# Kernel tuning notes

Hardware: AMD Instinct MI355X
Metric: run time of the kernel (lower is better)

The kernel has to match this reference:

```python
import jax, jax.numpy as jnp
import numpy as np

EPS_BN = 1e-5
EPS_NORM = 1e-12

def _proj(x, W, g, b, m, v):
    # x: (B,C,N); W: (O,C) 1x1 conv; eval-mode BN per out channel; ReLU
    y = jnp.einsum('oc,bcn->bon', W, x)
    s = g / jnp.sqrt(v + EPS_BN)
    y = (y - m[None, :, None]) * s[None, :, None] + b[None, :, None]
    return jax.nn.relu(y)

def _l2norm(x, axis):
    n = jnp.sqrt(jnp.sum(x * x, axis=axis, keepdims=True))
    return x / jnp.maximum(n, EPS_NORM)

def setup_inputs() -> dict:
    key = jax.random.key(0)
    ks = jax.random.split(key, 8)
    B, C, H, W = 8, 256, 96, 96
    NS, K = 256, 64  # num_state, K
    X = jax.random.normal(ks[0], (B, C, H, W), dtype=jnp.float32)
    def mk(k, out_c):
        return (jax.random.normal(k, (out_c, C), dtype=jnp.float32) * 0.05,
                jnp.ones((out_c,), jnp.float32), jnp.zeros((out_c,), jnp.float32),
                jnp.zeros((out_c,), jnp.float32), jnp.ones((out_c,), jnp.float32))
    phi_w, phi_g, phi_b, phi_m, phi_v = mk(ks[1], K)
    theta_w, theta_g, theta_b, theta_m, theta_v = mk(ks[2], NS)
    rou_w, rou_g, rou_b, rou_m, rou_v = mk(ks[3], NS)
    val_w, val_g, val_b, val_m, val_v = mk(ks[4], NS)
    return dict(X=X,
                phi_w=phi_w, phi_g=phi_g, phi_b=phi_b, phi_m=phi_m, phi_v=phi_v,
                theta_w=theta_w, theta_g=theta_g, theta_b=theta_b, theta_m=theta_m, theta_v=theta_v,
                rou_w=rou_w, rou_g=rou_g, rou_b=rou_b, rou_m=rou_m, rou_v=rou_v,
                val_w=val_w, val_g=val_g, val_b=val_b, val_m=val_m, val_v=val_v)

def reference(X, phi_w, phi_g, phi_b, phi_m, phi_v,
              theta_w, theta_g, theta_b, theta_m, theta_v,
              rou_w, rou_g, rou_b, rou_m, rou_v,
              val_w, val_g, val_b, val_m, val_v):
    B, C, H, W = X.shape
    N = H * W
    x = X.reshape(B, C, N)
    x_phi = _proj(x, phi_w, phi_g, phi_b, phi_m, phi_v)          # (B,K,N)
    x_theta = _proj(x, theta_w, theta_g, theta_b, theta_m, theta_v)  # (B,S,N)
    x_theta = jax.nn.softmax(x_theta, axis=-1)                   # softmax over N
    discrib = jnp.einsum('bkn,bsn->bks', x_phi, x_theta)         # (B,K,S)
    x_rou = _proj(x, rou_w, rou_g, rou_b, rou_m, rou_v)          # (B,S,N)
    x_rou = jax.nn.softmax(x_rou, axis=1)                        # softmax over channels S
    Q = jnp.einsum('bks,bsn->bnk', discrib, x_rou)               # (B,N,K)
    Q = _l2norm(Q, axis=1)                                       # F.normalize dim=1 (over N)
    Q = jax.nn.softmax(Q, axis=-1)                               # softmax over K
    x_val = _proj(x, val_w, val_g, val_b, val_m, val_v)          # (B,S,N)
    # Z = sum_n Q[b,n,k]*x_val[b,s,n] / sum_n Q[b,n,k]  -- batched GEMM, no (B,S,N,K) blowup
    Znum = jnp.einsum('bsn,bnk->bsk', x_val, Q)                  # (B,S,K)
    Z = Znum / Q.sum(axis=1)[:, None, :]
    Z = _l2norm(Z, axis=1)                                       # F.normalize dim=1 (over S)
    return (Z, Q)
```

## Files before the change

### kernel.cpp

```cpp
#include <hip/hip_runtime.h>
#include <math.h>

#define B_ 8
#define C_ 256
#define N_ 9216
#define S_ 256
#define K_ 64
#define NCHUNK 36
#define TILE_KS (K_ * S_)
#define NC8 (N_ / 8)

typedef unsigned short ushort_t;
typedef __attribute__((ext_vector_type(8))) short bf16x8;
typedef __attribute__((ext_vector_type(4))) float f32x4;

static __device__ inline ushort_t f2bf(float x) {
    unsigned int u = __float_as_uint(x);
    unsigned int r = (u + 0x7fffu + ((u >> 16) & 1u)) >> 16;
    return (ushort_t)r;
}
static __device__ inline float bf2f(ushort_t u) {
    return __uint_as_float(((unsigned int)u) << 16);
}

static __device__ inline uint4 expcell(uint4 u, float2 s) {
    uint4 r;
    unsigned int* up = (unsigned int*)&u;
    unsigned int* rp = (unsigned int*)&r;
#pragma unroll
    for (int q = 0; q < 4; ++q) {
        unsigned int x = up[q];
        float lo = __uint_as_float((x & 0xffffu) << 16);
        float hi = __uint_as_float(x & 0xffff0000u);
        float el = __expf(lo - s.x) * s.y;
        float eh = __expf(hi - s.x) * s.y;
        rp[q] = (unsigned int)f2bf(el) | ((unsigned int)f2bf(eh) << 16);
    }
    return r;
}

__global__ __launch_bounds__(256) void prep_w(
    const float* __restrict__ phi_w, const float* __restrict__ phi_g, const float* __restrict__ phi_b,
    const float* __restrict__ phi_m, const float* __restrict__ phi_v,
    const float* __restrict__ th_w, const float* __restrict__ th_g, const float* __restrict__ th_b,
    const float* __restrict__ th_m, const float* __restrict__ th_v,
    const float* __restrict__ ro_w, const float* __restrict__ ro_g, const float* __restrict__ ro_b,
    const float* __restrict__ ro_m, const float* __restrict__ ro_v,
    const float* __restrict__ va_w, const float* __restrict__ va_g, const float* __restrict__ va_b,
    const float* __restrict__ va_m, const float* __restrict__ va_v,
    ushort_t* __restrict__ Wt, float* __restrict__ be)
{
    const int o = blockIdx.x;
    const int t = threadIdx.x;
    const float *src, *g, *bb, *mm, *vv; int orel;
    if (o < 64)       { src = phi_w; g = phi_g; bb = phi_b; mm = phi_m; vv = phi_v; orel = o; }
    else if (o < 320) { src = th_w;  g = th_g;  bb = th_b;  mm = th_m;  vv = th_v;  orel = o - 64; }
    else if (o < 576) { src = ro_w;  g = ro_g;  bb = ro_b;  mm = ro_m;  vv = ro_v;  orel = o - 320; }
    else              { src = va_w;  g = va_g;  bb = va_b;  mm = va_m;  vv = va_v;  orel = o - 576; }
    const float s = g[orel] / sqrtf(vv[orel] + 1e-5f);
    const int ot = o >> 6, os = (o >> 4) & 3, st = t >> 5;
    const size_t flat = ((((size_t)ot * 8 + st) * 4 + os) * 64 + ((t >> 3) & 3) * 16 + (o & 15)) * 8 + (t & 7);
    Wt[flat] = f2bf(src[orel * C_ + t] * s);
    if (t == 0) be[o] = bb[orel] - mm[orel] * s;
}

__global__ __launch_bounds__(256) void xpose(
    const float* __restrict__ X, ushort_t* __restrict__ Xs)
{
    __shared__ float T[64][65];
    const int b = blockIdx.z, c0 = blockIdx.y * 64, n0 = blockIdx.x * 64;
    const int t = threadIdx.x;
#pragma unroll
    for (int p = 0; p < 4; ++p) {
        int c = p * 16 + (t >> 4), nn = (t & 15) * 4;
        float4 v = *(const float4*)&X[((size_t)b * C_ + c0 + c) * N_ + n0 + nn];
        T[c][nn] = v.x; T[c][nn + 1] = v.y; T[c][nn + 2] = v.z; T[c][nn + 3] = v.w;
    }
    __syncthreads();
#pragma unroll
    for (int p = 0; p < 4; ++p) {
        int nn = p * 16 + (t >> 4), cl = (t & 15) * 4;
        ushort4 u;
        u.x = f2bf(T[cl][nn]); u.y = f2bf(T[cl + 1][nn]);
        u.z = f2bf(T[cl + 2][nn]); u.w = f2bf(T[cl + 3][nn]);
        const int n = n0 + nn, c = c0 + cl;
        const int nt = n >> 8, nr = n & 255;
        const int st = c >> 5, g8 = (c >> 3) & 3, e = c & 7;
        const size_t base = ((((size_t)b * 36 + nt) * 8 + st) * 1024
                             + (nr >> 4) * 64 + g8 * 16 + (nr & 15)) * 8 + e;
        *(ushort4*)&Xs[base] = u;
    }
}

__global__ __launch_bounds__(256) void proj_mfma_all(
    const ushort_t* __restrict__ Wt, const float* __restrict__ be,
    const ushort_t* __restrict__ Xs,
    ushort_t* __restrict__ Pbf, ushort_t* __restrict__ Tbf,
    ushort_t* __restrict__ Vbf, ushort_t* __restrict__ Rt)
{
    __shared__ short sm[9216];
    const int t = threadIdx.x;
    const int l = t & 63, w = t >> 6;
    const int idx = blockIdx.x;
    const int xcd = idx & 7, pos = idx >> 3;
    const int vid = xcd * 468 + pos;
    const int ot  = vid % 13;
    const int r   = vid / 13;
    const int b   = r / 36;
    const int nt  = r % 36;
    const int n0  = nt * 256;
    const int o0  = ot * 64;

    const bf16x8* Wv = (const bf16x8*)Wt;
    const bf16x8* Xf = (const bf16x8*)Xs;
    const size_t xbase = ((size_t)b * 36 + nt) * 8192;
    const size_t wbase = (size_t)ot * 2048;
    const int boff = (l >> 4) * 16 + (l & 15);

    f32x4 zr = {0.f, 0.f, 0.f, 0.f};
    f32x4 acc[4][4];
#pragma unroll
    for (int i = 0; i < 4; ++i)
#pragma unroll
        for (int j = 0; j < 4; ++j) acc[i][j] = zr;

    bf16x8 A0[4], B0[4];
#pragma unroll
    for (int os = 0; os < 4; ++os) A0[os] = Wv[wbase + os * 64 + l];
#pragma unroll
    for (int j = 0; j < 4; ++j)   B0[j]  = Xf[xbase + (w * 4 + j) * 64 + boff];

#pragma unroll
    for (int st = 0; st < 8; ++st) {
        bf16x8 A1[4], B1[4];
        if (st < 7) {
#pragma unroll
            for (int os = 0; os < 4; ++os)
                A1[os] = Wv[wbase + (st + 1) * 256 + os * 64 + l];
#pragma unroll
            for (int j = 0; j < 4; ++j)
                B1[j] = Xf[xbase + (size_t)(st + 1) * 1024 + (w * 4 + j) * 64 + boff];
        }
#pragma unroll
        for (int os = 0; os < 4; ++os)
#pragma unroll
            for (int j = 0; j < 4; ++j)
                acc[os][j] = __builtin_amdgcn_mfma_f32_16x16x32_bf16(A0[os], B0[j], acc[os][j], 0, 0, 0);
#pragma unroll
        for (int os = 0; os < 4; ++os) A0[os] = A1[os];
#pragma unroll
        for (int j = 0; j < 4; ++j)   B0[j]  = B1[j];
    }

    if (o0 >= 320 && o0 < 576) {
        const int od = o0 - 320;
        ushort_t* Tt = (ushort_t*)sm + w * (32 * 72);
#pragma unroll
        for (int half = 0; half < 2; ++half) {
            __syncthreads();
#pragma unroll
            for (int jj = 0; jj < 2; ++jj) {
                const int j = half * 2 + jj;
#pragma unroll
                for (int os = 0; os < 4; ++os)
#pragma unroll
                    for (int r2 = 0; r2 < 4; ++r2) {
                        const int scol = os * 16 + (l >> 4) * 4 + r2;
                        const float bias = be[o0 + scol];
                        Tt[(jj * 16 + (l & 15)) * 72 + scol] = f2bf(fmaxf(acc[os][j][r2] + bias, 0.f));
                    }
            }
            __syncthreads();
#pragma unroll
            for (int p = 0; p < 4; ++p) {
                const int lrow = p * 8 + (l >> 3);
                uint4 v = *(const uint4*)&Tt[lrow * 72 + (l & 7) * 8];
                *(uint4*)&Rt[((size_t)b * N_ + n0 + w * 64 + half * 32 + lrow) * 256 + od + (l & 7) * 8] = v;
            }
        }
    } else {
        ushort_t* dst; int od, osz;
        if (o0 < 64)       { dst = Pbf; od = o0;       osz = 64;  }
        else if (o0 < 320) { dst = Tbf; od = o0 - 64;  osz = 256; }
        else               { dst = Vbf; od = o0 - 576; osz = 256; }
        ushort_t* Tw = (ushort_t*)sm + w * (32 * 68);
#pragma unroll
        for (int half = 0; half < 2; ++half) {
            __syncthreads();
#pragma unroll
            for (int osl = 0; osl < 2; ++osl) {
                const int os = half * 2 + osl;
#pragma unroll
                for (int r2 = 0; r2 < 4; ++r2) {
                    const int lrow = osl * 16 + (l >> 4) * 4 + r2;
                    const int orow = half * 32 + lrow;
                    const float bias = be[o0 + orow];
#pragma unroll
                    for (int j = 0; j < 4; ++j)
                        Tw[lrow * 68 + j * 16 + (l & 15)] = f2bf(fmaxf(acc[os][j][r2] + bias, 0.f));
                }
            }
            __syncthreads();
#pragma unroll
            for (int i = 0; i < 8; ++i) {
                const int lrow = i * 4 + (l >> 4);
                ushort4 v = *(const ushort4*)&Tw[lrow * 68 + (l & 15) * 4];
                *(ushort4*)&dst[((size_t)(b * osz + od + half * 32 + lrow)) * N_ + n0 + w * 64 + (l & 15) * 4] = v;
            }
        }
    }
}

__global__ __launch_bounds__(256) void rowstat_n(
    const ushort_t* __restrict__ T, float* __restrict__ st2)
{
    const int row = blockIdx.x;
    const ushort4* p = (const ushort4*)(T + (size_t)row * N_);
    const int t = threadIdx.x;
    float v[36];
    float mx = -INFINITY;
#pragma unroll
    for (int i = 0; i < 9; ++i) {
        ushort4 u = p[t + i * 256];
        v[i * 4 + 0] = bf2f(u.x); v[i * 4 + 1] = bf2f(u.y);
        v[i * 4 + 2] = bf2f(u.z); v[i * 4 + 3] = bf2f(u.w);
        mx = fmaxf(mx, fmaxf(fmaxf(v[i * 4], v[i * 4 + 1]), fmaxf(v[i * 4 + 2], v[i * 4 + 3])));
    }
    __shared__ float red[256];
    red[t] = mx; __syncthreads();
    for (int s2 = 128; s2 > 0; s2 >>= 1) {
        if (t < s2) red[t] = fmaxf(red[t], red[t + s2]);
        __syncthreads();
    }
    mx = red[0]; __syncthreads();
    float sum = 0.f;
#pragma unroll
    for (int i = 0; i < 36; ++i) sum += __expf(v[i] - mx);
    red[t] = sum; __syncthreads();
    for (int s2 = 128; s2 > 0; s2 >>= 1) {
        if (t < s2) red[t] += red[t + s2];
        __syncthreads();
    }
    if (t == 0) ((float2*)st2)[row] = make_float2(mx, 1.0f / red[0]);
}

__global__ __launch_bounds__(256) void softmax_rows(ushort_t* __restrict__ R)
{
    const int w = threadIdx.x >> 6, l = threadIdx.x & 63;
    const size_t row0 = (size_t)blockIdx.x * 32 + w * 8;
    for (int r = 0; r < 8; ++r) {
        ushort4* p = (ushort4*)(R + (row0 + r) * 256);
        ushort4 u = p[l];
        float f0 = bf2f(u.x), f1 = bf2f(u.y), f2 = bf2f(u.z), f3 = bf2f(u.w);
        float mx = fmaxf(fmaxf(f0, f1), fmaxf(f2, f3));
#pragma unroll
        for (int m = 1; m < 64; m <<= 1) mx = fmaxf(mx, __shfl_xor(mx, m));
        f0 = __expf(f0 - mx); f1 = __expf(f1 - mx); f2 = __expf(f2 - mx); f3 = __expf(f3 - mx);
        float s = f0 + f1 + f2 + f3;
#pragma unroll
        for (int m = 1; m < 64; m <<= 1) s += __shfl_xor(s, m);
        const float inv = 1.0f / s;
        u.x = f2bf(f0 * inv); u.y = f2bf(f1 * inv); u.z = f2bf(f2 * inv); u.w = f2bf(f3 * inv);
        p[l] = u;
    }
}

__global__ __launch_bounds__(256) void ks_mfma(
    const ushort_t* __restrict__ A, const ushort_t* __restrict__ Bm,
    const float* __restrict__ st2, float* __restrict__ P)
{
    __shared__ short sm[32768];
    const int t = threadIdx.x;
    const int l = t & 63, w = t >> 6;
    const int chunk = blockIdx.x, b = blockIdx.y;
    const int ccell = chunk * 32;

    const uint4* Av = (const uint4*)A;
    const uint4* Bv = (const uint4*)Bm;
    const float2* S2 = (const float2*)st2;
    uint4* smv = (uint4*)sm;
    const bool doexp = (st2 != nullptr);

    uint4 wreg[8], xreg[8];
    float2 sreg[8];
#pragma unroll
    for (int i = 0; i < 8; ++i) {
        int cell = i * 256 + t;
        int osub = cell >> 9, g = (cell >> 4) & 31, oi = cell & 15;
        wreg[i] = Av[(size_t)(b * 64 + osub * 16 + oi) * NC8 + ccell + g];
    }
#pragma unroll
    for (int i = 0; i < 8; ++i) {
        int cell = i * 256 + t;
        int s = cell >> 7, g8 = (cell >> 4) & 7, ni = cell & 15;
        int row = s * 16 + ni;
        xreg[i] = Bv[(size_t)(b * 256 + row) * NC8 + ccell + g8];
        if (doexp) sreg[i] = S2[b * 256 + row];
    }
#pragma unroll
    for (int i = 0; i < 8; ++i) smv[i * 256 + t] = wreg[i];
#pragma unroll
    for (int i = 0; i < 8; ++i) smv[2048 + i * 256 + t] = doexp ? expcell(xreg[i], sreg[i]) : xreg[i];
    __syncthreads();

    f32x4 zr = {0.f, 0.f, 0.f, 0.f};
    f32x4 acc[4][4];
#pragma unroll
    for (int i = 0; i < 4; ++i)
#pragma unroll
        for (int j = 0; j < 4; ++j) acc[i][j] = zr;

    const bf16x8* smW = (const bf16x8*)sm;
    const bf16x8* smX = (const bf16x8*)(sm + 16384);

    for (int st = 0; st < 4; ++st) {
        if (st < 3) {
#pragma unroll
            for (int i = 0; i < 8; ++i) {
                int cell = i * 256 + t;
                int s = cell >> 7, g8 = (cell >> 4) & 7, ni = cell & 15;
                int row = s * 16 + ni;
                xreg[i] = Bv[(size_t)(b * 256 + row) * NC8 + ccell + (st + 1) * 8 + g8];
                if (doexp) sreg[i] = S2[b * 256 + row];
            }
        }
#pragma unroll
        for (int kgl = 0; kgl < 2; ++kgl) {
            const int kg = st * 2 + kgl;
            bf16x8 Af[4], Bf[4];
#pragma unroll
            for (int os = 0; os < 4; ++os)
                Af[os] = smW[(os * 32 + kg * 4 + (l >> 4)) * 16 + (l & 15)];
#pragma unroll
            for (int j = 0; j < 4; ++j)
                Bf[j] = smX[((w * 4 + j) * 8 + kgl * 4 + (l >> 4)) * 16 + (l & 15)];
#pragma unroll
            for (int os = 0; os < 4; ++os)
#pragma unroll
                for (int j = 0; j < 4; ++j)
                    acc[os][j] = __builtin_amdgcn_mfma_f32_16x16x32_bf16(Af[os], Bf[j], acc[os][j], 0, 0, 0);
        }
        __syncthreads();
        if (st < 3) {
#pragma unroll
            for (int i = 0; i < 8; ++i) smv[2048 + i * 256 + t] = doexp ? expcell(xreg[i], sreg[i]) : xreg[i];
            __syncthreads();
        }
    }

    float* Pb = P + ((size_t)(chunk * B_ + b)) * TILE_KS;
#pragma unroll
    for (int os = 0; os < 4; ++os)
#pragma unroll
        for (int r = 0; r < 4; ++r) {
            const int k = os * 16 + (l >> 4) * 4 + r;
#pragma unroll
            for (int j = 0; j < 4; ++j)
                Pb[k * 256 + (w * 4 + j) * 16 + (l & 15)] = acc[os][j][r];
        }
}

__global__ __launch_bounds__(256) void qt_mfma(
    const ushort_t* __restrict__ Dbf,
    const ushort_t* __restrict__ Rsm,
    float* __restrict__ Qraw,
    float* __restrict__ Nrm)
{
    __shared__ short sm[32768];
    const int t = threadIdx.x;
    const int l = t & 63, w = t >> 6;
    const int b = blockIdx.x / 36;
    const int n0 = (blockIdx.x % 36) * 256;

    const uint4* Av = (const uint4*)Dbf;
    const uint4* Xv = (const uint4*)Rsm;
    uint4* smv = (uint4*)sm;

    uint4 wreg[8], xreg[8];
#pragma unroll
    for (int i = 0; i < 8; ++i) {
        int cell = i * 256 + t;
        int osub = cell >> 9, g = (cell >> 4) & 31, oi = cell & 15;
        wreg[i] = Av[(size_t)(b * 64 + osub * 16 + oi) * 32 + g];
    }
#pragma unroll
    for (int i = 0; i < 8; ++i) {
        int cell = i * 256 + t;
        int s = cell >> 7, g8 = (cell >> 4) & 7, ni = cell & 15;
        xreg[i] = Xv[((size_t)b * N_ + n0 + s * 16 + ni) * 32 + g8];
    }
#pragma unroll
    for (int i = 0; i < 8; ++i) smv[i * 256 + t] = wreg[i];
#pragma unroll
    for (int i = 0; i < 8; ++i) smv[2048 + i * 256 + t] = xreg[i];
    __syncthreads();

    f32x4 zr = {0.f, 0.f, 0.f, 0.f};
    f32x4 acc[4][4];
#pragma unroll
    for (int i = 0; i < 4; ++i)
#pragma unroll
        for (int j = 0; j < 4; ++j) acc[i][j] = zr;

    const bf16x8* smW = (const bf16x8*)sm;
    const bf16x8* smX = (const bf16x8*)(sm + 16384);

    for (int st = 0; st < 4; ++st) {
        if (st < 3) {
#pragma unroll
            for (int i = 0; i < 8; ++i) {
                int cell = i * 256 + t;
                int s = cell >> 7, g8 = (cell >> 4) & 7, ni = cell & 15;
                xreg[i] = Xv[((size_t)b * N_ + n0 + s * 16 + ni) * 32 + (st + 1) * 8 + g8];
            }
        }
#pragma unroll
        for (int kgl = 0; kgl < 2; ++kgl) {
            const int kg = st * 2 + kgl;
            bf16x8 Af[4], Bf[4];
#pragma unroll
            for (int os = 0; os < 4; ++os)
                Af[os] = smW[(os * 32 + kg * 4 + (l >> 4)) * 16 + (l & 15)];
#pragma unroll
            for (int j = 0; j < 4; ++j)
                Bf[j] = smX[((w * 4 + j) * 8 + kgl * 4 + (l >> 4)) * 16 + (l & 15)];
#pragma unroll
            for (int os = 0; os < 4; ++os)
#pragma unroll
                for (int j = 0; j < 4; ++j)
                    acc[os][j] = __builtin_amdgcn_mfma_f32_16x16x32_bf16(Af[os], Bf[j], acc[os][j], 0, 0, 0);
        }
        __syncthreads();
        if (st < 3) {
#pragma unroll
            for (int i = 0; i < 8; ++i) smv[2048 + i * 256 + t] = xreg[i];
            __syncthreads();
        }
    }

    float* snrm = (float*)sm + 9216;
    __syncthreads();
    if (t < 64) snrm[t] = 0.f;
    __syncthreads();
#pragma unroll
    for (int os = 0; os < 4; ++os)
#pragma unroll
        for (int r = 0; r < 4; ++r) {
            float p = 0.f;
#pragma unroll
            for (int j = 0; j < 4; ++j) p = fmaf(acc[os][j][r], acc[os][j][r], p);
#pragma unroll
            for (int m = 1; m < 16; m <<= 1) p += __shfl_xor(p, m);
            if ((l & 15) == 0) atomicAdd(&snrm[os * 16 + (l >> 4) * 4 + r], p);
        }
    float* Tw = (float*)sm + w * 2304;
#pragma unroll
    for (int h = 0; h < 2; ++h) {
        __syncthreads();
#pragma unroll
        for (int os = 0; os < 4; ++os)
#pragma unroll
            for (int r = 0; r < 4; ++r) {
                const int kcol = os * 16 + (l >> 4) * 4 + r;
#pragma unroll
                for (int jj = 0; jj < 2; ++jj)
                    Tw[(jj * 16 + (l & 15)) * 72 + kcol] = acc[os][h * 2 + jj][r];
            }
        __syncthreads();
#pragma unroll
        for (int i = 0; i < 8; ++i) {
            const int lrow = i * 4 + (l >> 4);
            f32x4 v = *(const f32x4*)&Tw[lrow * 72 + (l & 15) * 4];
            *(f32x4*)&Qraw[((size_t)b * N_ + n0 + w * 64 + h * 32 + lrow) * 64 + (l & 15) * 4] = v;
        }
    }
    __syncthreads();
    if (t < 64) atomicAdd(&Nrm[b * 64 + t], snrm[t]);
}

__global__ __launch_bounds__(256) void chunk_reduce_bf(
    const float* __restrict__ P, ushort_t* __restrict__ outb)
{
    const int i = blockIdx.x * 256 + threadIdx.x;
    float s = 0.f;
#pragma unroll
    for (int c = 0; c < NCHUNK; ++c) s += P[(size_t)c * (B_ * TILE_KS) + i];
    outb[i] = f2bf(s);
}
__global__ __launch_bounds__(256) void chunk_reduce_f(
    const float* __restrict__ P, float* __restrict__ outf)
{
    const int i = blockIdx.x * 256 + threadIdx.x;
    float s = 0.f;
#pragma unroll
    for (int c = 0; c < NCHUNK; ++c) s += P[(size_t)c * (B_ * TILE_KS) + i];
    outf[i] = s;
}

__global__ __launch_bounds__(256) void q_final(
    const float* __restrict__ Qraw, const float* __restrict__ Nrm,
    float* __restrict__ Qout, ushort_t* __restrict__ Qbf)
{
    __shared__ ushort_t Tq[64 * 256];
    __shared__ float invn[64];
    const int b = blockIdx.y;
    const int n0 = blockIdx.x * 256;
    const int t = threadIdx.x;
    const int l = t & 63, w = t >> 6;
    if (t < 64) invn[t] = 1.0f / fmaxf(sqrtf(Nrm[b * 64 + t]), 1e-12f);
    __syncthreads();
    const size_t base = ((size_t)b * N_ + n0 + t) * 64;
    float q[64];
#pragma unroll
    for (int kk = 0; kk < 16; ++kk) {
        f32x4 v = *(const f32x4*)&Qraw[base + kk * 4];
        q[kk * 4 + 0] = v[0]; q[kk * 4 + 1] = v[1]; q[kk * 4 + 2] = v[2]; q[kk * 4 + 3] = v[3];
    }
    float mx = -INFINITY;
#pragma unroll
    for (int k = 0; k < 64; ++k) { q[k] *= invn[k]; mx = fmaxf(mx, q[k]); }
    float sum = 0.f;
#pragma unroll
    for (int k = 0; k < 64; ++k) { q[k] = __expf(q[k] - mx); sum += q[k]; }
    const float inv = 1.0f / sum;
#pragma unroll
    for (int kk = 0; kk < 16; ++kk) {
        f32x4 v = {q[kk * 4] * inv, q[kk * 4 + 1] * inv, q[kk * 4 + 2] * inv, q[kk * 4 + 3] * inv};
        *(f32x4*)&Qout[base + kk * 4] = v;
        q[kk * 4] = v[0]; q[kk * 4 + 1] = v[1]; q[kk * 4 + 2] = v[2]; q[kk * 4 + 3] = v[3];
    }
#pragma unroll
    for (int k = 0; k < 64; ++k) Tq[k * 256 + t] = f2bf(q[k]);
    __syncthreads();
#pragma unroll
    for (int kk = 0; kk < 16; ++kk) {
        const int k = kk * 4 + w;
        ushort4 v = *(const ushort4*)&Tq[k * 256 + l * 4];
        *(ushort4*)&Qbf[((size_t)b * 64 + k) * N_ + n0 + l * 4] = v;
    }
}

__global__ __launch_bounds__(256) void z_final(
    const float* __restrict__ ZnT, float* __restrict__ Z)
{
    __shared__ float red[256];
    __shared__ float invn[64];
    const int b = blockIdx.x;
    const int t = threadIdx.x;
    const float* Zb = ZnT + (size_t)b * TILE_KS;
    {
        const int k = t >> 2, qq = t & 3;
        float ss = 0.f;
        for (int j = 0; j < 64; ++j) {
            float v = Zb[k * 256 + qq * 64 + j];
            ss = fmaf(v, v, ss);
        }
        red[t] = ss;
    }
    __syncthreads();
    if ((t & 3) == 0) {
        float tot = red[t] + red[t + 1] + red[t + 2] + red[t + 3];
        invn[t >> 2] = 1.0f / fmaxf(sqrtf(tot), 1e-12f);
    }
    __syncthreads();
    {
        const int k = t & 63, w = t >> 6;
        const float sc = invn[k];
        for (int j = 0; j < 64; ++j) {
            int s = w * 64 + j;
            Z[((size_t)b * 256 + s) * 64 + k] = Zb[k * 256 + s] * sc;
        }
    }
}

extern "C" void kernel_launch(void* const* d_in, const int* in_sizes, int n_in,
                              void* d_out, int out_size, void* d_ws, size_t ws_size,
                              hipStream_t stream)
{
    const float* X       = (const float*)d_in[0];
    const float* phi_w   = (const float*)d_in[1];
    const float* phi_g   = (const float*)d_in[2];
    const float* phi_b   = (const float*)d_in[3];
    const float* phi_m   = (const float*)d_in[4];
    const float* phi_v   = (const float*)d_in[5];
    const float* theta_w = (const float*)d_in[6];
    const float* theta_g = (const float*)d_in[7];
    const float* theta_b = (const float*)d_in[8];
    const float* theta_m = (const float*)d_in[9];
    const float* theta_v = (const float*)d_in[10];
    const float* rou_w   = (const float*)d_in[11];
    const float* rou_g   = (const float*)d_in[12];
    const float* rou_b   = (const float*)d_in[13];
    const float* rou_m   = (const float*)d_in[14];
    const float* rou_v   = (const float*)d_in[15];
    const float* val_w   = (const float*)d_in[16];
    const float* val_g   = (const float*)d_in[17];
    const float* val_b   = (const float*)d_in[18];
    const float* val_m   = (const float*)d_in[19];
    const float* val_v   = (const float*)d_in[20];

    float* ws = (float*)d_ws;
    size_t off = 0;
    ushort_t* Xs  = (ushort_t*)(ws + off); off += (size_t)B_ * N_ * C_ / 2;
    ushort_t* Wt  = (ushort_t*)(ws + off); off += 832 * C_ / 2;
    float* be     = ws + off; off += 832;
    float* st2    = ws + off; off += 2 * B_ * 256;
    ushort_t* Pbf = (ushort_t*)(ws + off); off += (size_t)B_ * 64 * N_ / 2;
    ushort_t* Tbf = (ushort_t*)(ws + off); off += (size_t)B_ * 256 * N_ / 2;
    ushort_t* Vbf = (ushort_t*)(ws + off); off += (size_t)B_ * 256 * N_ / 2;
    ushort_t* Rt  = (ushort_t*)(ws + off); off += (size_t)B_ * N_ * 256 / 2;
    ushort_t* Qbf = (ushort_t*)(ws + off); off += (size_t)B_ * 64 * N_ / 2;
    ushort_t* Dbf = (ushort_t*)(ws + off); off += (size_t)B_ * 64 * 256 / 2;
    float* part   = ws + off; off += (size_t)NCHUNK * B_ * TILE_KS;
    float* Qraw   = ws + off; off += (size_t)B_ * N_ * 64;
    float* ZnT    = ws + off; off += (size_t)B_ * TILE_KS;
    float* Nrm    = ws + off; off += B_ * 64;

    float* Zout = (float*)d_out;
    float* Qout = Zout + (size_t)B_ * S_ * K_;

    hipMemsetAsync(Nrm, 0, B_ * 64 * sizeof(float), stream);

    prep_w<<<832, 256, 0, stream>>>(phi_w, phi_g, phi_b, phi_m, phi_v,
                                    theta_w, theta_g, theta_b, theta_m, theta_v,
                                    rou_w, rou_g, rou_b, rou_m, rou_v,
                                    val_w, val_g, val_b, val_m, val_v, Wt, be);
    xpose<<<dim3(N_ / 64, C_ / 64, B_), 256, 0, stream>>>(X, Xs);

    proj_mfma_all<<<3744, 256, 0, stream>>>(Wt, be, Xs, Pbf, Tbf, Vbf, Rt);

    rowstat_n<<<B_ * 256, 256, 0, stream>>>(Tbf, st2);
    softmax_rows<<<B_ * N_ / 32, 256, 0, stream>>>(Rt);

    ks_mfma<<<dim3(NCHUNK, B_), 256, 0, stream>>>(Pbf, Tbf, st2, part);
    chunk_reduce_bf<<<B_ * TILE_KS / 256, 256, 0, stream>>>(part, Dbf);

    qt_mfma<<<36 * B_, 256, 0, stream>>>(Dbf, Rt, Qraw, Nrm);
    q_final<<<dim3(36, B_), 256, 0, stream>>>(Qraw, Nrm, Qout, Qbf);

    ks_mfma<<<dim3(NCHUNK, B_), 256, 0, stream>>>(Qbf, Vbf, (const float*)nullptr, part);
    chunk_reduce_f<<<B_ * TILE_KS / 256, 256, 0, stream>>>(part, ZnT);
    z_final<<<B_, 256, 0, stream>>>(ZnT, Zout);
}
```

Before: 233.1 us.

## Defer channel softmax into qt_mfma, use packed bf16 converts, vectorize chunk reductions

The channel softmax over Rt is split: a new rowstat_rt kernel writes only per-row max and reciprocal-sum, and qt_mfma applies exp and scale while staging tiles into shared memory, so the normalized bf16 write-back of Rt is gone. Scalar bf16 rounding is replaced by the hardware packed v_cvt_pk_bf16_f32 instruction in xpose, the projection epilogues and expcell. The chunk_reduce kernels now handle four elements per thread with float4 loads. The trade is extra exp work inside qt_mfma, an added per-row stats buffer, and one fewer rounding step for the softmax values.

```diff
diff --git a/kernel.cpp b/kernel.cpp
--- a/kernel.cpp
+++ b/kernel.cpp
@@ -22,6 +22,11 @@
 static __device__ inline float bf2f(ushort_t u) {
     return __uint_as_float(((unsigned int)u) << 16);
 }
+static __device__ inline unsigned int cvtpk(float lo, float hi) {
+    unsigned int r;
+    asm("v_cvt_pk_bf16_f32 %0, %1, %2" : "=v"(r) : "v"(lo), "v"(hi));
+    return r;
+}
 
 static __device__ inline uint4 expcell(uint4 u, float2 s) {
     uint4 r;
@@ -32,9 +37,7 @@
         unsigned int x = up[q];
         float lo = __uint_as_float((x & 0xffffu) << 16);
         float hi = __uint_as_float(x & 0xffff0000u);
-        float el = __expf(lo - s.x) * s.y;
-        float eh = __expf(hi - s.x) * s.y;
-        rp[q] = (unsigned int)f2bf(el) | ((unsigned int)f2bf(eh) << 16);
+        rp[q] = cvtpk(__expf(lo - s.x) * s.y, __expf(hi - s.x) * s.y);
     }
     return r;
 }
@@ -80,15 +83,15 @@
 #pragma unroll
     for (int p = 0; p < 4; ++p) {
         int nn = p * 16 + (t >> 4), cl = (t & 15) * 4;
-        ushort4 u;
-        u.x = f2bf(T[cl][nn]); u.y = f2bf(T[cl + 1][nn]);
-        u.z = f2bf(T[cl + 2][nn]); u.w = f2bf(T[cl + 3][nn]);
+        uint2 uu;
+        uu.x = cvtpk(T[cl][nn], T[cl + 1][nn]);
+        uu.y = cvtpk(T[cl + 2][nn], T[cl + 3][nn]);
         const int n = n0 + nn, c = c0 + cl;
         const int nt = n >> 8, nr = n & 255;
         const int st = c >> 5, g8 = (c >> 3) & 3, e = c & 7;
         const size_t base = ((((size_t)b * 36 + nt) * 8 + st) * 1024
                              + (nr >> 4) * 64 + g8 * 16 + (nr & 15)) * 8 + e;
-        *(ushort4*)&Xs[base] = u;
+        *(uint2*)&Xs[base] = uu;
     }
 }
 
@@ -161,14 +164,19 @@
 #pragma unroll
             for (int jj = 0; jj < 2; ++jj) {
                 const int j = half * 2 + jj;
-#pragma unroll
-                for (int os = 0; os < 4; ++os)
-#pragma unroll
-                    for (int r2 = 0; r2 < 4; ++r2) {
-                        const int scol = os * 16 + (l >> 4) * 4 + r2;
-                        const float bias = be[o0 + scol];
-                        Tt[(jj * 16 + (l & 15)) * 72 + scol] = f2bf(fmaxf(acc[os][j][r2] + bias, 0.f));
-                    }
+                const int row = jj * 16 + (l & 15);
+#pragma unroll
+                for (int os = 0; os < 4; ++os) {
+                    const int scol0 = os * 16 + (l >> 4) * 4;
+                    const float b0 = be[o0 + scol0], b1 = be[o0 + scol0 + 1];
+                    const float b2 = be[o0 + scol0 + 2], b3 = be[o0 + scol0 + 3];
+                    unsigned int p0 = cvtpk(fmaxf(acc[os][j][0] + b0, 0.f),
+                                            fmaxf(acc[os][j][1] + b1, 0.f));
+                    unsigned int p1 = cvtpk(fmaxf(acc[os][j][2] + b2, 0.f),
+                                            fmaxf(acc[os][j][3] + b3, 0.f));
+                    *(unsigned int*)&Tt[row * 72 + scol0]     = p0;
+                    *(unsigned int*)&Tt[row * 72 + scol0 + 2] = p1;
+                }
             }
             __syncthreads();
 #pragma unroll
@@ -184,6 +192,7 @@
         else if (o0 < 320) { dst = Tbf; od = o0 - 64;  osz = 256; }
         else               { dst = Vbf; od = o0 - 576; osz = 256; }
         ushort_t* Tw = (ushort_t*)sm + w * (32 * 68);
+        const int c = l & 15;
 #pragma unroll
         for (int half = 0; half < 2; ++half) {
             __syncthreads();
@@ -195,9 +204,14 @@
                     const int lrow = osl * 16 + (l >> 4) * 4 + r2;
                     const int orow = half * 32 + lrow;
                     const float bias = be[o0 + orow];
-#pragma unroll
-                    for (int j = 0; j < 4; ++j)
-                        Tw[lrow * 68 + j * 16 + (l & 15)] = f2bf(fmaxf(acc[os][j][r2] + bias, 0.f));
+                    unsigned int p0 = cvtpk(fmaxf(acc[os][0][r2] + bias, 0.f),
+                                            fmaxf(acc[os][1][r2] + bias, 0.f));
+                    unsigned int p1 = cvtpk(fmaxf(acc[os][2][r2] + bias, 0.f),
+                                            fmaxf(acc[os][3][r2] + bias, 0.f));
+                    Tw[lrow * 68 + c]      = (ushort_t)p0;
+                    Tw[lrow * 68 + 16 + c] = (ushort_t)(p0 >> 16);
+                    Tw[lrow * 68 + 32 + c] = (ushort_t)p1;
+                    Tw[lrow * 68 + 48 + c] = (ushort_t)(p1 >> 16);
                 }
             }
             __syncthreads();
@@ -244,24 +258,22 @@
     if (t == 0) ((float2*)st2)[row] = make_float2(mx, 1.0f / red[0]);
 }
 
-__global__ __launch_bounds__(256) void softmax_rows(ushort_t* __restrict__ R)
+__global__ __launch_bounds__(256) void rowstat_rt(
+    const ushort_t* __restrict__ R, float* __restrict__ st2r)
 {
     const int w = threadIdx.x >> 6, l = threadIdx.x & 63;
     const size_t row0 = (size_t)blockIdx.x * 32 + w * 8;
     for (int r = 0; r < 8; ++r) {
-        ushort4* p = (ushort4*)(R + (row0 + r) * 256);
+        const ushort4* p = (const ushort4*)(R + (row0 + r) * 256);
         ushort4 u = p[l];
         float f0 = bf2f(u.x), f1 = bf2f(u.y), f2 = bf2f(u.z), f3 = bf2f(u.w);
         float mx = fmaxf(fmaxf(f0, f1), fmaxf(f2, f3));
 #pragma unroll
         for (int m = 1; m < 64; m <<= 1) mx = fmaxf(mx, __shfl_xor(mx, m));
-        f0 = __expf(f0 - mx); f1 = __expf(f1 - mx); f2 = __expf(f2 - mx); f3 = __expf(f3 - mx);
-        float s = f0 + f1 + f2 + f3;
+        float s = __expf(f0 - mx) + __expf(f1 - mx) + __expf(f2 - mx) + __expf(f3 - mx);
 #pragma unroll
         for (int m = 1; m < 64; m <<= 1) s += __shfl_xor(s, m);
-        const float inv = 1.0f / s;
-        u.x = f2bf(f0 * inv); u.y = f2bf(f1 * inv); u.z = f2bf(f2 * inv); u.w = f2bf(f3 * inv);
-        p[l] = u;
+        if (l == 0) ((float2*)st2r)[row0 + r] = make_float2(mx, 1.0f / s);
     }
 }
 
@@ -321,7 +333,6 @@
                 int s = cell >> 7, g8 = (cell >> 4) & 7, ni = cell & 15;
                 int row = s * 16 + ni;
                 xreg[i] = Bv[(size_t)(b * 256 + row) * NC8 + ccell + (st + 1) * 8 + g8];
-                if (doexp) sreg[i] = S2[b * 256 + row];
             }
         }
 #pragma unroll
@@ -362,7 +373,8 @@
 
 __global__ __launch_bounds__(256) void qt_mfma(
     const ushort_t* __restrict__ Dbf,
-    const ushort_t* __restrict__ Rsm,
+    const ushort_t* __restrict__ Rraw,
+    const float* __restrict__ st2r,
     float* __restrict__ Qraw,
     float* __restrict__ Nrm)
 {
@@ -373,10 +385,12 @@
     const int n0 = (blockIdx.x % 36) * 256;
 
     const uint4* Av = (const uint4*)Dbf;
-    const uint4* Xv = (const uint4*)Rsm;
+    const uint4* Xv = (const uint4*)Rraw;
+    const float2* S2 = (const float2*)st2r;
     uint4* smv = (uint4*)sm;
 
     uint4 wreg[8], xreg[8];
+    float2 sreg[8];
 #pragma unroll
     for (int i = 0; i < 8; ++i) {
         int cell = i * 256 + t;
@@ -388,11 +402,12 @@
         int cell = i * 256 + t;
         int s = cell >> 7, g8 = (cell >> 4) & 7, ni = cell & 15;
         xreg[i] = Xv[((size_t)b * N_ + n0 + s * 16 + ni) * 32 + g8];
+        sreg[i] = S2[(size_t)b * N_ + n0 + s * 16 + ni];
     }
 #pragma unroll
     for (int i = 0; i < 8; ++i) smv[i * 256 + t] = wreg[i];
 #pragma unroll
-    for (int i = 0; i < 8; ++i) smv[2048 + i * 256 + t] = xreg[i];
+    for (int i = 0; i < 8; ++i) smv[2048 + i * 256 + t] = expcell(xreg[i], sreg[i]);
     __syncthreads();
 
     f32x4 zr = {0.f, 0.f, 0.f, 0.f};
@@ -433,7 +448,7 @@
         __syncthreads();
         if (st < 3) {
 #pragma unroll
-            for (int i = 0; i < 8; ++i) smv[2048 + i * 256 + t] = xreg[i];
+            for (int i = 0; i < 8; ++i) smv[2048 + i * 256 + t] = expcell(xreg[i], sreg[i]);
             __syncthreads();
         }
     }
@@ -481,20 +496,29 @@
 __global__ __launch_bounds__(256) void chunk_reduce_bf(
     const float* __restrict__ P, ushort_t* __restrict__ outb)
 {
-    const int i = blockIdx.x * 256 + threadIdx.x;
-    float s = 0.f;
-#pragma unroll
-    for (int c = 0; c < NCHUNK; ++c) s += P[(size_t)c * (B_ * TILE_KS) + i];
-    outb[i] = f2bf(s);
+    const int i4 = blockIdx.x * 256 + threadIdx.x;
+    float4 s = make_float4(0.f, 0.f, 0.f, 0.f);
+#pragma unroll
+    for (int c = 0; c < NCHUNK; ++c) {
+        float4 v = ((const float4*)P)[(size_t)c * (B_ * TILE_KS / 4) + i4];
+        s.x += v.x; s.y += v.y; s.z += v.z; s.w += v.w;
+    }
+    uint2 uu;
+    uu.x = cvtpk(s.x, s.y);
+    uu.y = cvtpk(s.z, s.w);
+    ((uint2*)outb)[i4] = uu;
 }
 __global__ __launch_bounds__(256) void chunk_reduce_f(
     const float* __restrict__ P, float* __restrict__ outf)
 {
-    const int i = blockIdx.x * 256 + threadIdx.x;
-    float s = 0.f;
-#pragma unroll
-    for (int c = 0; c < NCHUNK; ++c) s += P[(size_t)c * (B_ * TILE_KS) + i];
-    outf[i] = s;
+    const int i4 = blockIdx.x * 256 + threadIdx.x;
+    float4 s = make_float4(0.f, 0.f, 0.f, 0.f);
+#pragma unroll
+    for (int c = 0; c < NCHUNK; ++c) {
+        float4 v = ((const float4*)P)[(size_t)c * (B_ * TILE_KS / 4) + i4];
+        s.x += v.x; s.y += v.y; s.z += v.z; s.w += v.w;
+    }
+    ((float4*)outf)[i4] = s;
 }
 
 __global__ __launch_bounds__(256) void q_final(
@@ -605,6 +629,7 @@
     ushort_t* Wt  = (ushort_t*)(ws + off); off += 832 * C_ / 2;
     float* be     = ws + off; off += 832;
     float* st2    = ws + off; off += 2 * B_ * 256;
+    float* st2r   = ws + off; off += 2 * B_ * N_;
     ushort_t* Pbf = (ushort_t*)(ws + off); off += (size_t)B_ * 64 * N_ / 2;
     ushort_t* Tbf = (ushort_t*)(ws + off); off += (size_t)B_ * 256 * N_ / 2;
     ushort_t* Vbf = (ushort_t*)(ws + off); off += (size_t)B_ * 256 * N_ / 2;
@@ -630,15 +655,15 @@
     proj_mfma_all<<<3744, 256, 0, stream>>>(Wt, be, Xs, Pbf, Tbf, Vbf, Rt);
 
     rowstat_n<<<B_ * 256, 256, 0, stream>>>(Tbf, st2);
-    softmax_rows<<<B_ * N_ / 32, 256, 0, stream>>>(Rt);
+    rowstat_rt<<<B_ * N_ / 32, 256, 0, stream>>>(Rt, st2r);
 
     ks_mfma<<<dim3(NCHUNK, B_), 256, 0, stream>>>(Pbf, Tbf, st2, part);
-    chunk_reduce_bf<<<B_ * TILE_KS / 256, 256, 0, stream>>>(part, Dbf);
-
-    qt_mfma<<<36 * B_, 256, 0, stream>>>(Dbf, Rt, Qraw, Nrm);
+    chunk_reduce_bf<<<B_ * TILE_KS / 1024, 256, 0, stream>>>(part, Dbf);
+
+    qt_mfma<<<36 * B_, 256, 0, stream>>>(Dbf, Rt, st2r, Qraw, Nrm);
     q_final<<<dim3(36, B_), 256, 0, stream>>>(Qraw, Nrm, Qout, Qbf);
 
     ks_mfma<<<dim3(NCHUNK, B_), 256, 0, stream>>>(Qbf, Vbf, (const float*)nullptr, part);
-    chunk_reduce_f<<<B_ * TILE_KS / 256, 256, 0, stream>>>(part, ZnT);
+    chunk_reduce_f<<<B_ * TILE_KS / 1024, 256, 0, stream>>>(part, ZnT);
     z_final<<<B_, 256, 0, stream>>>(ZnT, Zout);
 }
```

Result: faster. 201.4 us, median of 2 (-13.6%).
